# Optimization experiments

Measured on AMD Instinct MI355X. Metric: run time of the kernel, lower is better.

## Reference

```python
import jax, jax.numpy as jnp
import numpy as np

LAMB_MAX = 2.0


def cheb_conv_k2(x, edge_index, w0, w1, b):
    """PyG ChebConv with K=2, sym normalization, given lambda_max.
    out = x @ w0 + (L_hat x) @ w1 + b, where
    L_hat = (2/lmax) * (I - D^{-1/2} A D^{-1/2}) - I.
    """
    n = x.shape[0]
    src, dst = edge_index[0], edge_index[1]
    ew = jnp.ones(src.shape, x.dtype)
    deg = jax.ops.segment_sum(ew, src, num_segments=n)
    dinv = jnp.where(deg > 0, jax.lax.rsqrt(jnp.maximum(deg, 1e-12)), 0.0)
    s = 2.0 / LAMB_MAX
    # off-diagonal weights of scaled Laplacian: -s * d_i^{-1/2} d_j^{-1/2}
    norm = (-s) * dinv[src] * dinv[dst]  # [E]
    # gather-scale-scatter: (L_hat x)_offdiag
    agg = jax.ops.segment_sum(norm[:, None] * x[src], dst, num_segments=n)  # [N, F]
    tx1 = (s - 1.0) * x + agg  # diagonal: s*1 (L diag) + (-1) self-loop
    return x @ w0 + tx1 @ w1 + b


def setup_inputs() -> dict:
    key = jax.random.key(0)
    ks = jax.random.split(key, 8)
    N, E, F, H = 100000, 1600000, 128, 128
    x = jax.random.normal(ks[0], (N, F), dtype=jnp.float32)
    edge_index = jax.random.randint(ks[1], (2, E), 0, N, dtype=jnp.int32)
    # glorot-ish init for the two Chebyshev linear weights per layer
    sc1 = (2.0 / (F + H)) ** 0.5
    sc2 = (2.0 / (H + 1)) ** 0.5
    w1_0 = jax.random.normal(ks[2], (F, H), dtype=jnp.float32) * sc1
    w1_1 = jax.random.normal(ks[3], (F, H), dtype=jnp.float32) * sc1
    b1 = jnp.zeros((H,), jnp.float32)
    w2_0 = jax.random.normal(ks[4], (H, 1), dtype=jnp.float32) * sc2
    w2_1 = jax.random.normal(ks[5], (H, 1), dtype=jnp.float32) * sc2
    b2 = jnp.zeros((1,), jnp.float32)
    return {"x": x, "edge_index": edge_index, "w1_0": w1_0, "w1_1": w1_1,
            "b1": b1, "w2_0": w2_0, "w2_1": w2_1, "b2": b2}


def reference(x, edge_index, w1_0, w1_1, b1, w2_0, w2_1, b2):
    h = jax.nn.relu(cheb_conv_k2(x, edge_index, w1_0, w1_1, b1))
    out = jax.nn.sigmoid(cheb_conv_k2(h, edge_index, w2_0, w2_1, b2))
    return out  # [N, 1]
```

## Files before the change

kernel.cpp:

```cpp
#include <hip/hip_runtime.h>
#include <math.h>

#define F 128
#define SCAN_CHUNK 1024
#define CHUNK 32
#define NBLK 128

typedef __attribute__((ext_vector_type(8))) short bf16x8;
typedef __attribute__((ext_vector_type(4))) float f32x4;

__device__ inline unsigned short f2bf(float v) {
  unsigned u = __float_as_uint(v);
  unsigned r = (u + 0x7FFFu + ((u >> 16) & 1u)) >> 16;
  return (unsigned short)r;
}
__device__ inline float bf2f(unsigned short s) {
  return __uint_as_float(((unsigned)s) << 16);
}

__global__ __launch_bounds__(256) void k_conv(const float* __restrict__ x,
                                              unsigned short* __restrict__ xb,
                                              int NF4) {
  const float4* x4 = (const float4*)x;
  ushort4* xb4 = (ushort4*)xb;
  for (int i = blockIdx.x * 256 + threadIdx.x; i < NF4; i += gridDim.x * 256) {
    float4 v = x4[i];
    ushort4 o;
    o.x = f2bf(v.x);
    o.y = f2bf(v.y);
    o.z = f2bf(v.z);
    o.w = f2bf(v.w);
    xb4[i] = o;
  }
}

__global__ __launch_bounds__(1024) void k_hist2(const int* __restrict__ src,
                                                const int* __restrict__ dst,
                                                int* __restrict__ cntgD,
                                                int* __restrict__ cntgS, int E,
                                                int nb, int per) {
  extern __shared__ int smem[];
  int* cd = smem;
  int* cs = smem + nb;
  int blk = blockIdx.x;
  for (int b = threadIdx.x; b < nb; b += 1024) {
    cd[b] = 0;
    cs[b] = 0;
  }
  __syncthreads();
  int e0 = blk * per;
  int e1 = e0 + per;
  if (e1 > E) e1 = E;
  for (int e = e0 + threadIdx.x; e < e1; e += 1024) {
    atomicAdd(&cd[dst[e] >> 7], 1);
    atomicAdd(&cs[src[e] >> 7], 1);
  }
  __syncthreads();
  for (int b = threadIdx.x; b < nb; b += 1024) {
    cntgD[b * NBLK + blk] = cd[b];
    cntgS[b * NBLK + blk] = cs[b];
  }
}

__global__ __launch_bounds__(NBLK) void k_scanBk2(int* __restrict__ cntgD,
                                                  int* __restrict__ cntgS,
                                                  int* __restrict__ totD,
                                                  int* __restrict__ totS, int nb) {
  __shared__ int sh[NBLK];
  int b = blockIdx.x;
  int tid = threadIdx.x;
  int* cntg;
  int* tot;
  int bb;
  if (b < nb) {
    cntg = cntgD;
    tot = totD;
    bb = b;
  } else {
    cntg = cntgS;
    tot = totS;
    bb = b - nb;
  }
  int v = cntg[bb * NBLK + tid];
  int val = v;
  sh[tid] = val;
  __syncthreads();
  for (int off = 1; off < NBLK; off <<= 1) {
    int o = (tid >= off) ? sh[tid - off] : 0;
    __syncthreads();
    val += o;
    sh[tid] = val;
    __syncthreads();
  }
  cntg[bb * NBLK + tid] = val - v;
  if (tid == NBLK - 1) tot[bb] = val;
}

__global__ __launch_bounds__(1024) void k_scanTot(const int* __restrict__ totD,
                                                  const int* __restrict__ totS,
                                                  int* __restrict__ baseD,
                                                  int* __restrict__ baseS, int nb,
                                                  int E) {
  __shared__ int sh[1024];
  int tid = threadIdx.x;
  int v = (tid < nb) ? totD[tid] : 0;
  int val = v;
  sh[tid] = val;
  __syncthreads();
  for (int off = 1; off < 1024; off <<= 1) {
    int o = (tid >= off) ? sh[tid - off] : 0;
    __syncthreads();
    val += o;
    sh[tid] = val;
    __syncthreads();
  }
  if (tid < nb) baseD[tid] = val - v;
  if (tid == 0) baseD[nb] = E;
  __syncthreads();
  v = (tid < nb) ? totS[tid] : 0;
  val = v;
  sh[tid] = val;
  __syncthreads();
  for (int off = 1; off < 1024; off <<= 1) {
    int o = (tid >= off) ? sh[tid - off] : 0;
    __syncthreads();
    val += o;
    sh[tid] = val;
    __syncthreads();
  }
  if (tid < nb) baseS[tid] = val - v;
  if (tid == 0) baseS[nb] = E;
}

__global__ __launch_bounds__(1024) void k_binfill2(
    const int* __restrict__ src, const int* __restrict__ dst,
    const int* __restrict__ cntgD, const int* __restrict__ cntgS,
    const int* __restrict__ baseD, const int* __restrict__ baseS,
    unsigned* __restrict__ binnedD, unsigned char* __restrict__ binnedS, int E,
    int nb, int per) {
  extern __shared__ int smem[];
  int* bD = smem;
  int* cD = smem + nb;
  int* bS = smem + 2 * nb;
  int* cS = smem + 3 * nb;
  int blk = blockIdx.x;
  for (int b = threadIdx.x; b < nb; b += 1024) {
    bD[b] = baseD[b] + cntgD[b * NBLK + blk];
    cD[b] = 0;
    bS[b] = baseS[b] + cntgS[b * NBLK + blk];
    cS[b] = 0;
  }
  __syncthreads();
  int e0 = blk * per;
  int e1 = e0 + per;
  if (e1 > E) e1 = E;
  for (int e = e0 + threadIdx.x; e < e1; e += 1024) {
    int s = src[e];
    int d = dst[e];
    int bk = d >> 7;
    int rk = atomicAdd(&cD[bk], 1);
    binnedD[bD[bk] + rk] = ((unsigned)s << 7) | (unsigned)(d & 127);
    int bs = s >> 7;
    int rs = atomicAdd(&cS[bs], 1);
    binnedS[bS[bs] + rs] = (unsigned char)(s & 127);
  }
}

__global__ __launch_bounds__(256) void k_dinvS(const unsigned char* __restrict__ binnedS,
                                               const int* __restrict__ baseS,
                                               float* __restrict__ dinv, int N) {
  __shared__ int cnt[128];
  int b = blockIdx.x;
  int tid = threadIdx.x;
  if (tid < 128) cnt[tid] = 0;
  int wbeg = baseS[b], wend = baseS[b + 1];
  __syncthreads();
  for (int j = wbeg + tid; j < wend; j += 256) atomicAdd(&cnt[binnedS[j]], 1);
  __syncthreads();
  if (tid < 128) {
    int node = (b << 7) + tid;
    if (node < N) {
      int c = cnt[tid];
      dinv[node] = c > 0 ? rsqrtf((float)c) : 0.0f;
    }
  }
}

__global__ __launch_bounds__(256) void k_binB2(const unsigned* __restrict__ binnedD,
                                               const int* __restrict__ baseD,
                                               int* __restrict__ rp,
                                               int* __restrict__ pairs, int N,
                                               int E) {
  __shared__ int cnt[128];
  __shared__ int sc[256];
  __shared__ int cur[128];
  int b = blockIdx.x;
  int tid = threadIdx.x;
  int node0 = b << 7;
  if (tid < 128) cnt[tid] = 0;
  int wbeg = baseD[b], wend = baseD[b + 1];
  __syncthreads();
  for (int j = wbeg + tid; j < wend; j += 256) atomicAdd(&cnt[binnedD[j] & 127u], 1);
  __syncthreads();
  int v = (tid < 128) ? cnt[tid] : 0;
  int val = v;
  sc[tid] = val;
  __syncthreads();
  for (int off = 1; off < 128; off <<= 1) {
    int o = (tid >= off) ? sc[tid - off] : 0;
    __syncthreads();
    val += o;
    sc[tid] = val;
    __syncthreads();
  }
  if (tid < 128) {
    int excl = wbeg + val - v;
    int node = node0 + tid;
    if (node < N) rp[node] = excl;
    cur[tid] = excl;
  }
  if (b == 0 && tid == 0) rp[N] = E;
  __syncthreads();
  for (int j = wbeg + tid; j < wend; j += 256) {
    unsigned e = binnedD[j];
    int idx = atomicAdd(&cur[e & 127u], 1);
    pairs[idx] = (int)(e >> 7);
  }
}

__global__ __launch_bounds__(256) void k_prep(const int* __restrict__ src,
                                              const int* __restrict__ dst,
                                              const float* __restrict__ x,
                                              int* __restrict__ degA,
                                              int* __restrict__ degB,
                                              unsigned short* __restrict__ xb,
                                              int E, int NF4) {
  int t0 = blockIdx.x * 256 + threadIdx.x;
  int stride = gridDim.x * 256;
  for (int i = t0; i < E; i += stride) {
    atomicAdd(&degA[src[i]], 1);
    atomicAdd(&degB[dst[i]], 1);
  }
  const float4* x4 = (const float4*)x;
  ushort4* xb4 = (ushort4*)xb;
  for (int i = t0; i < NF4; i += stride) {
    float4 v = x4[i];
    ushort4 o;
    o.x = f2bf(v.x);
    o.y = f2bf(v.y);
    o.z = f2bf(v.z);
    o.w = f2bf(v.w);
    xb4[i] = o;
  }
}

__global__ __launch_bounds__(256) void k_scanA(const int* __restrict__ deg,
                                               int* __restrict__ rp,
                                               int* __restrict__ bsum, int N) {
  __shared__ int sh[256];
  int tid = threadIdx.x;
  int base = blockIdx.x * SCAN_CHUNK + tid * 4;
  int v0 = 0, v1 = 0, v2 = 0, v3 = 0;
  if (base + 0 < N) v0 = deg[base + 0];
  if (base + 1 < N) v1 = deg[base + 1];
  if (base + 2 < N) v2 = deg[base + 2];
  if (base + 3 < N) v3 = deg[base + 3];
  int ts = v0 + v1 + v2 + v3;
  int val = ts;
  sh[tid] = val;
  __syncthreads();
  for (int off = 1; off < 256; off <<= 1) {
    int other = (tid >= off) ? sh[tid - off] : 0;
    __syncthreads();
    val += other;
    sh[tid] = val;
    __syncthreads();
  }
  int excl = val - ts;
  if (base + 0 < N) rp[base + 0] = excl;
  if (base + 1 < N) rp[base + 1] = excl + v0;
  if (base + 2 < N) rp[base + 2] = excl + v0 + v1;
  if (base + 3 < N) rp[base + 3] = excl + v0 + v1 + v2;
  if (tid == 255) bsum[blockIdx.x] = val;
}

__global__ __launch_bounds__(256) void k_scanB(int* __restrict__ bsum, int nb) {
  __shared__ int sh[256];
  int tid = threadIdx.x;
  int ts = (tid < nb) ? bsum[tid] : 0;
  int val = ts;
  sh[tid] = val;
  __syncthreads();
  for (int off = 1; off < 256; off <<= 1) {
    int other = (tid >= off) ? sh[tid - off] : 0;
    __syncthreads();
    val += other;
    sh[tid] = val;
    __syncthreads();
  }
  if (tid < nb) bsum[tid] = val - ts;
}

__global__ __launch_bounds__(256) void k_scanC(int* __restrict__ rp,
                                               const int* __restrict__ bsum,
                                               int* __restrict__ pos,
                                               const int* __restrict__ degA,
                                               float* __restrict__ dinv, int N,
                                               int E) {
  int i = blockIdx.x * 256 + threadIdx.x;
  if (i < N) {
    int v = rp[i] + bsum[i >> 10];
    rp[i] = v;
    pos[i] = v;
    int d = degA[i];
    dinv[i] = d > 0 ? rsqrtf((float)d) : 0.0f;
  }
  if (i == 0) rp[N] = E;
}

__global__ __launch_bounds__(256) void k_fill(const int* __restrict__ src,
                                              const int* __restrict__ dst,
                                              int* __restrict__ pos,
                                              int* __restrict__ pairs, int E) {
  for (int e = blockIdx.x * 256 + threadIdx.x; e < E; e += gridDim.x * 256) {
    int s = src[e];
    int d = dst[e];
    int idx = atomicAdd(&pos[d], 1);
    pairs[idx] = s;
  }
}

__global__ __launch_bounds__(256) void k_gather1b(
    const int* __restrict__ pairs, const int* __restrict__ rp,
    const unsigned short* __restrict__ xb, const float* __restrict__ dinv,
    unsigned short* __restrict__ tb, int N) {
  int node = (blockIdx.x * 256 + threadIdx.x) >> 6;
  if (node >= N) return;
  int lane = threadIdx.x & 63;
  int half = lane >> 5;
  int li = lane & 31;
  int beg = rp[node], end = rp[node + 1];
  const uint2* x2 = (const uint2*)xb;
  float a0 = 0.f, a1 = 0.f, a2 = 0.f, a3 = 0.f;
  int j = beg + half;
  for (; j + 2 < end; j += 4) {
    int s0 = pairs[j];
    int s1 = pairs[j + 2];
    float w0 = dinv[s0];
    float w1 = dinv[s1];
    uint2 v0 = x2[(size_t)s0 * 32 + li];
    uint2 v1 = x2[(size_t)s1 * 32 + li];
    a0 += w0 * bf2f((unsigned short)v0.x) + w1 * bf2f((unsigned short)v1.x);
    a1 += w0 * bf2f((unsigned short)(v0.x >> 16)) +
          w1 * bf2f((unsigned short)(v1.x >> 16));
    a2 += w0 * bf2f((unsigned short)v0.y) + w1 * bf2f((unsigned short)v1.y);
    a3 += w0 * bf2f((unsigned short)(v0.y >> 16)) +
          w1 * bf2f((unsigned short)(v1.y >> 16));
  }
  for (; j < end; j += 2) {
    int s0 = pairs[j];
    float w0 = dinv[s0];
    uint2 v0 = x2[(size_t)s0 * 32 + li];
    a0 += w0 * bf2f((unsigned short)v0.x);
    a1 += w0 * bf2f((unsigned short)(v0.x >> 16));
    a2 += w0 * bf2f((unsigned short)v0.y);
    a3 += w0 * bf2f((unsigned short)(v0.y >> 16));
  }
  a0 += __shfl_xor(a0, 32);
  a1 += __shfl_xor(a1, 32);
  a2 += __shfl_xor(a2, 32);
  a3 += __shfl_xor(a3, 32);
  if (half == 0) {
    float nd = -dinv[node];
    uint2 o;
    o.x = ((unsigned)f2bf(nd * a1) << 16) | f2bf(nd * a0);
    o.y = ((unsigned)f2bf(nd * a3) << 16) | f2bf(nd * a2);
    ((uint2*)tb)[(size_t)node * 32 + li] = o;
  }
}

__global__ __launch_bounds__(256) void k_layer_mfma(
    const float* __restrict__ x, const unsigned short* __restrict__ tb,
    const float* __restrict__ dinv, const float* __restrict__ w10,
    const float* __restrict__ w11, const float* __restrict__ b1,
    const float* __restrict__ w20, const float* __restrict__ w21,
    float* __restrict__ p, float* __restrict__ r, int N) {
  __shared__ __align__(16) short Axh[8 * 16 * 40];
  __shared__ __align__(16) short Axl[8 * 16 * 40];
  __shared__ __align__(16) short At[8 * 16 * 40];
  __shared__ float p_sh[CHUNK], r_sh[CHUNK];

  const int tid = threadIdx.x;
  const int wave = tid >> 6;
  const int lane = tid & 63;
  const int quad = lane >> 4;
  const int col = lane & 15;

  bf16x8 Bh[2][4][2], Bl[2][4][2];
  float b1f[2], w20f[2], w21f[2];
#pragma unroll
  for (int nt = 0; nt < 2; ++nt) {
    int f = wave * 32 + nt * 16 + col;
    b1f[nt] = b1[f];
    w20f[nt] = w20[f];
    w21f[nt] = w21[f];
  }
#pragma unroll
  for (int mat = 0; mat < 2; ++mat) {
    const float* w = mat ? w11 : w10;
#pragma unroll
    for (int ks = 0; ks < 4; ++ks) {
#pragma unroll
      for (int nt = 0; nt < 2; ++nt) {
        int f = wave * 32 + nt * 16 + col;
        bf16x8 h8, l8;
#pragma unroll
        for (int j = 0; j < 8; ++j) {
          float v = w[(ks * 32 + quad * 8 + j) * F + f];
          unsigned short hi = f2bf(v);
          l8[j] = (short)f2bf(v - bf2f(hi));
          h8[j] = (short)hi;
        }
        Bh[mat][ks][nt] = h8;
        Bl[mat][ks][nt] = l8;
      }
    }
  }

  const int nchunks = (N + CHUNK - 1) / CHUNK;
  for (int chunk = blockIdx.x; chunk < nchunks; chunk += gridDim.x) {
    int node0 = chunk * CHUNK;
    __syncthreads();

    {
      int nloc = tid >> 3;
      int k0 = (tid & 7) * 16;
      int gn = node0 + nloc;
      int mt = nloc >> 4, m = nloc & 15, ks = k0 >> 5, koff = k0 & 31;
      int base = ((mt * 4 + ks) * 16 + m) * 40 + koff;
      const float4* xr = (const float4*)(x + (size_t)gn * F + k0);
      const uint2* tr = (const uint2*)(tb + (size_t)gn * F + k0);
      bool ok = (gn < N);
#pragma unroll
      for (int q4 = 0; q4 < 4; ++q4) {
        float4 xv = ok ? xr[q4] : make_float4(0.f, 0.f, 0.f, 0.f);
        uint2 tv = ok ? tr[q4] : make_uint2(0u, 0u);
        short4 xh, xl;
        unsigned short h;
        h = f2bf(xv.x); xl.x = (short)f2bf(xv.x - bf2f(h)); xh.x = (short)h;
        h = f2bf(xv.y); xl.y = (short)f2bf(xv.y - bf2f(h)); xh.y = (short)h;
        h = f2bf(xv.z); xl.z = (short)f2bf(xv.z - bf2f(h)); xh.z = (short)h;
        h = f2bf(xv.w); xl.w = (short)f2bf(xv.w - bf2f(h)); xh.w = (short)h;
        *(short4*)&Axh[base + q4 * 4] = xh;
        *(short4*)&Axl[base + q4 * 4] = xl;
        *(uint2*)&At[base + q4 * 4] = tv;
      }
      if (tid < CHUNK) {
        p_sh[tid] = 0.f;
        r_sh[tid] = 0.f;
      }
    }
    __syncthreads();

    f32x4 acc[2][2];
#pragma unroll
    for (int mt = 0; mt < 2; ++mt)
#pragma unroll
      for (int nt = 0; nt < 2; ++nt) acc[mt][nt] = (f32x4)0.f;

#pragma unroll
    for (int mt = 0; mt < 2; ++mt) {
#pragma unroll
      for (int ks = 0; ks < 4; ++ks) {
        int ab = ((mt * 4 + ks) * 16 + col) * 40 + quad * 8;
        bf16x8 axh = *(bf16x8*)&Axh[ab];
        bf16x8 axl = *(bf16x8*)&Axl[ab];
        bf16x8 at = *(bf16x8*)&At[ab];
#pragma unroll
        for (int nt = 0; nt < 2; ++nt) {
          f32x4 c = acc[mt][nt];
          c = __builtin_amdgcn_mfma_f32_16x16x32_bf16(axh, Bh[0][ks][nt], c, 0, 0, 0);
          c = __builtin_amdgcn_mfma_f32_16x16x32_bf16(axl, Bh[0][ks][nt], c, 0, 0, 0);
          c = __builtin_amdgcn_mfma_f32_16x16x32_bf16(axh, Bl[0][ks][nt], c, 0, 0, 0);
          c = __builtin_amdgcn_mfma_f32_16x16x32_bf16(at, Bh[1][ks][nt], c, 0, 0, 0);
          c = __builtin_amdgcn_mfma_f32_16x16x32_bf16(at, Bl[1][ks][nt], c, 0, 0, 0);
          acc[mt][nt] = c;
        }
      }
    }

#pragma unroll
    for (int mt = 0; mt < 2; ++mt) {
      float pp[4], rr[4];
#pragma unroll
      for (int reg = 0; reg < 4; ++reg) {
        float h0 = fmaxf(acc[mt][0][reg] + b1f[0], 0.f);
        float h1 = fmaxf(acc[mt][1][reg] + b1f[1], 0.f);
        pp[reg] = h0 * w20f[0] + h1 * w20f[1];
        rr[reg] = h0 * w21f[0] + h1 * w21f[1];
      }
#pragma unroll
      for (int off = 1; off < 16; off <<= 1) {
#pragma unroll
        for (int reg = 0; reg < 4; ++reg) {
          pp[reg] += __shfl_xor(pp[reg], off);
          rr[reg] += __shfl_xor(rr[reg], off);
        }
      }
      if (col == 0) {
#pragma unroll
        for (int reg = 0; reg < 4; ++reg) {
          atomicAdd(&p_sh[mt * 16 + quad * 4 + reg], pp[reg]);
          atomicAdd(&r_sh[mt * 16 + quad * 4 + reg], rr[reg]);
        }
      }
    }
    __syncthreads();
    if (tid < CHUNK) {
      int gn = node0 + tid;
      if (gn < N) {
        p[gn] = p_sh[tid];
        r[gn] = dinv[gn] * r_sh[tid];
      }
    }
  }
}

__global__ __launch_bounds__(256) void k_gather2_final(
    const int* __restrict__ pairs, const int* __restrict__ rp,
    const float* __restrict__ r2, const float* __restrict__ p,
    const float* __restrict__ dinv, const float* __restrict__ b2,
    float* __restrict__ out, int N) {
  int i = blockIdx.x * 256 + threadIdx.x;
  if (i >= N) return;
  int beg = rp[i], end = rp[i + 1];
  float a = 0.f;
  for (int j = beg; j < end; ++j) a += r2[pairs[j]];
  float z = p[i] - dinv[i] * a + b2[0];
  out[i] = 1.0f / (1.0f + expf(-z));
}

extern "C" void kernel_launch(void* const* d_in, const int* in_sizes, int n_in,
                              void* d_out, int out_size, void* d_ws, size_t ws_size,
                              hipStream_t stream) {
  const float* x = (const float*)d_in[0];
  const int* ei = (const int*)d_in[1];
  const float* w10 = (const float*)d_in[2];
  const float* w11 = (const float*)d_in[3];
  const float* b1 = (const float*)d_in[4];
  const float* w20 = (const float*)d_in[5];
  const float* w21 = (const float*)d_in[6];
  const float* b2 = (const float*)d_in[7];
  float* out = (float*)d_out;
  int N = in_sizes[0] / F;
  int E = in_sizes[1] / 2;
  const int* src = ei;
  const int* dst = ei + E;
  int nbuckets = (N + 127) >> 7;

  size_t off = 0;
  char* base = (char*)d_ws;
  auto take = [&](size_t bytes) {
    void* ptr = base + off;
    off += (bytes + 15) & ~(size_t)15;
    return ptr;
  };
  float* dinv = (float*)take((size_t)N * 4);
  float* p = (float*)take((size_t)N * 4);
  float* r = (float*)take((size_t)N * 4);
  int* rp = (int*)take(((size_t)N + 1) * 4);
  int* degA = (int*)take((size_t)N * 4);
  int* degB = (int*)take((size_t)N * 4);
  int* pos = (int*)take((size_t)N * 4);
  int* bsum = (int*)take(256 * 4);
  int* cntgD = (int*)take((size_t)nbuckets * NBLK * 4);
  int* cntgS = (int*)take((size_t)nbuckets * NBLK * 4);
  int* totD = (int*)take(((size_t)nbuckets + 1) * 4);
  int* totS = (int*)take(((size_t)nbuckets + 1) * 4);
  int* baseD = (int*)take(((size_t)nbuckets + 1) * 4);
  int* baseS = (int*)take(((size_t)nbuckets + 1) * 4);
  int* pairs = (int*)take((size_t)E * 4);
  unsigned short* xb = (unsigned short*)take((size_t)N * F * 2);
  unsigned short* tb = (unsigned short*)take((size_t)N * F * 2);
  if (off > ws_size) return;
  unsigned* binnedD = (unsigned*)tb;
  unsigned char* binnedS = (unsigned char*)tb + (((size_t)E * 4 + 255) & ~(size_t)255);

  int NF4 = N * (F / 4);
  int per = (E + NBLK - 1) / NBLK;

  k_conv<<<2048, 256, 0, stream>>>(x, xb, NF4);
  if (nbuckets <= 1024 && (size_t)E * 5 + 256 <= (size_t)N * F * 2) {
    k_hist2<<<NBLK, 1024, (size_t)nbuckets * 8, stream>>>(src, dst, cntgD, cntgS, E,
                                                          nbuckets, per);
    k_scanBk2<<<2 * nbuckets, NBLK, 0, stream>>>(cntgD, cntgS, totD, totS, nbuckets);
    k_scanTot<<<1, 1024, 0, stream>>>(totD, totS, baseD, baseS, nbuckets, E);
    k_binfill2<<<NBLK, 1024, (size_t)nbuckets * 16, stream>>>(
        src, dst, cntgD, cntgS, baseD, baseS, binnedD, binnedS, E, nbuckets, per);
    k_dinvS<<<nbuckets, 256, 0, stream>>>(binnedS, baseS, dinv, N);
    k_binB2<<<nbuckets, 256, 0, stream>>>(binnedD, baseD, rp, pairs, N, E);
  } else {
    int nb_scan = (N + SCAN_CHUNK - 1) / SCAN_CHUNK;
    hipMemsetAsync(degA, 0, 2 * (size_t)N * sizeof(int), stream);
    k_prep<<<2048, 256, 0, stream>>>(src, dst, x, degA, degB, xb, E, NF4);
    k_scanA<<<nb_scan, 256, 0, stream>>>(degB, rp, bsum, N);
    k_scanB<<<1, 256, 0, stream>>>(bsum, nb_scan);
    k_scanC<<<(N + 255) / 256, 256, 0, stream>>>(rp, bsum, pos, degA, dinv, N, E);
    k_fill<<<2048, 256, 0, stream>>>(src, dst, pos, pairs, E);
  }
  k_gather1b<<<(N + 3) / 4, 256, 0, stream>>>(pairs, rp, xb, dinv, tb, N);
  k_layer_mfma<<<512, 256, 0, stream>>>(x, tb, dinv, w10, w11, b1, w20, w21, p, r,
                                        N);
  k_gather2_final<<<(N + 255) / 256, 256, 0, stream>>>(pairs, rp, r, p, dinv, b2,
                                                       out, N);
}
```

Before: 326.9 us.

## Fuse prep kernels, drop split-bf16 x path, and re-map first gather

Folds the fp32-to-bf16 conversion of x into the histogram kernel, and merges the degree/dinv computation into the CSR-building kernel, removing two launches and one pass over the binned data. The layer MFMA kernel now reads the bf16 copy of x rather than fp32 x, and drops the hi/lo split of x. This cuts global traffic and MFMA work per tile, at the cost of lower precision on the x@w0 term. The first gather now uses 32 lanes per node with a 4-edge unroll instead of two half-waves plus a shuffle reduction, which is meant to raise memory-level parallelism.

```diff
diff --git a/kernel.cpp b/kernel.cpp
--- a/kernel.cpp
+++ b/kernel.cpp
@@ -18,12 +18,33 @@
   return __uint_as_float(((unsigned)s) << 16);
 }
 
-__global__ __launch_bounds__(256) void k_conv(const float* __restrict__ x,
-                                              unsigned short* __restrict__ xb,
-                                              int NF4) {
+__global__ __launch_bounds__(1024) void k_prep2(const int* __restrict__ src,
+                                                const int* __restrict__ dst,
+                                                const float* __restrict__ x,
+                                                unsigned short* __restrict__ xb,
+                                                int* __restrict__ cntgD,
+                                                int* __restrict__ cntgS, int E,
+                                                int NF4, int nb, int per) {
+  extern __shared__ int smem[];
+  int* cd = smem;
+  int* cs = smem + nb;
+  int blk = blockIdx.x;
+  int tid = threadIdx.x;
+  for (int b = tid; b < nb; b += 1024) {
+    cd[b] = 0;
+    cs[b] = 0;
+  }
+  __syncthreads();
+  int e0 = blk * per;
+  int e1 = e0 + per;
+  if (e1 > E) e1 = E;
+  for (int e = e0 + tid; e < e1; e += 1024) {
+    atomicAdd(&cd[dst[e] >> 7], 1);
+    atomicAdd(&cs[src[e] >> 7], 1);
+  }
   const float4* x4 = (const float4*)x;
   ushort4* xb4 = (ushort4*)xb;
-  for (int i = blockIdx.x * 256 + threadIdx.x; i < NF4; i += gridDim.x * 256) {
+  for (int i = blk * 1024 + tid; i < NF4; i += NBLK * 1024) {
     float4 v = x4[i];
     ushort4 o;
     o.x = f2bf(v.x);
@@ -32,31 +53,8 @@
     o.w = f2bf(v.w);
     xb4[i] = o;
   }
-}
-
-__global__ __launch_bounds__(1024) void k_hist2(const int* __restrict__ src,
-                                                const int* __restrict__ dst,
-                                                int* __restrict__ cntgD,
-                                                int* __restrict__ cntgS, int E,
-                                                int nb, int per) {
-  extern __shared__ int smem[];
-  int* cd = smem;
-  int* cs = smem + nb;
-  int blk = blockIdx.x;
-  for (int b = threadIdx.x; b < nb; b += 1024) {
-    cd[b] = 0;
-    cs[b] = 0;
-  }
-  __syncthreads();
-  int e0 = blk * per;
-  int e1 = e0 + per;
-  if (e1 > E) e1 = E;
-  for (int e = e0 + threadIdx.x; e < e1; e += 1024) {
-    atomicAdd(&cd[dst[e] >> 7], 1);
-    atomicAdd(&cs[src[e] >> 7], 1);
-  }
-  __syncthreads();
-  for (int b = threadIdx.x; b < nb; b += 1024) {
+  __syncthreads();
+  for (int b = tid; b < nb; b += 1024) {
     cntgD[b * NBLK + blk] = cd[b];
     cntgS[b * NBLK + blk] = cs[b];
   }
@@ -166,31 +164,13 @@
   }
 }
 
-__global__ __launch_bounds__(256) void k_dinvS(const unsigned char* __restrict__ binnedS,
-                                               const int* __restrict__ baseS,
-                                               float* __restrict__ dinv, int N) {
-  __shared__ int cnt[128];
-  int b = blockIdx.x;
-  int tid = threadIdx.x;
-  if (tid < 128) cnt[tid] = 0;
-  int wbeg = baseS[b], wend = baseS[b + 1];
-  __syncthreads();
-  for (int j = wbeg + tid; j < wend; j += 256) atomicAdd(&cnt[binnedS[j]], 1);
-  __syncthreads();
-  if (tid < 128) {
-    int node = (b << 7) + tid;
-    if (node < N) {
-      int c = cnt[tid];
-      dinv[node] = c > 0 ? rsqrtf((float)c) : 0.0f;
-    }
-  }
-}
-
-__global__ __launch_bounds__(256) void k_binB2(const unsigned* __restrict__ binnedD,
-                                               const int* __restrict__ baseD,
-                                               int* __restrict__ rp,
-                                               int* __restrict__ pairs, int N,
-                                               int E) {
+__global__ __launch_bounds__(256) void k_csr(const unsigned char* __restrict__ binnedS,
+                                             const int* __restrict__ baseS,
+                                             const unsigned* __restrict__ binnedD,
+                                             const int* __restrict__ baseD,
+                                             float* __restrict__ dinv,
+                                             int* __restrict__ rp,
+                                             int* __restrict__ pairs, int N, int E) {
   __shared__ int cnt[128];
   __shared__ int sc[256];
   __shared__ int cur[128];
@@ -198,8 +178,20 @@
   int tid = threadIdx.x;
   int node0 = b << 7;
   if (tid < 128) cnt[tid] = 0;
+  __syncthreads();
+  int sbeg = baseS[b], send = baseS[b + 1];
+  for (int j = sbeg + tid; j < send; j += 256) atomicAdd(&cnt[binnedS[j]], 1);
+  __syncthreads();
+  if (tid < 128) {
+    int node = node0 + tid;
+    if (node < N) {
+      int c = cnt[tid];
+      dinv[node] = c > 0 ? rsqrtf((float)c) : 0.0f;
+    }
+    cnt[tid] = 0;
+  }
+  __syncthreads();
   int wbeg = baseD[b], wend = baseD[b + 1];
-  __syncthreads();
   for (int j = wbeg + tid; j < wend; j += 256) atomicAdd(&cnt[binnedD[j] & 127u], 1);
   __syncthreads();
   int v = (tid < 128) ? cnt[tid] : 0;
@@ -330,34 +322,38 @@
   }
 }
 
-__global__ __launch_bounds__(256) void k_gather1b(
+__global__ __launch_bounds__(256) void k_gather1c(
     const int* __restrict__ pairs, const int* __restrict__ rp,
     const unsigned short* __restrict__ xb, const float* __restrict__ dinv,
     unsigned short* __restrict__ tb, int N) {
-  int node = (blockIdx.x * 256 + threadIdx.x) >> 6;
+  int node = (blockIdx.x * 256 + threadIdx.x) >> 5;
   if (node >= N) return;
-  int lane = threadIdx.x & 63;
-  int half = lane >> 5;
-  int li = lane & 31;
+  int li = threadIdx.x & 31;
   int beg = rp[node], end = rp[node + 1];
   const uint2* x2 = (const uint2*)xb;
   float a0 = 0.f, a1 = 0.f, a2 = 0.f, a3 = 0.f;
-  int j = beg + half;
-  for (; j + 2 < end; j += 4) {
-    int s0 = pairs[j];
-    int s1 = pairs[j + 2];
-    float w0 = dinv[s0];
-    float w1 = dinv[s1];
+  int j = beg;
+  for (; j + 3 < end; j += 4) {
+    int s0 = pairs[j], s1 = pairs[j + 1], s2 = pairs[j + 2], s3 = pairs[j + 3];
+    float w0 = dinv[s0], w1 = dinv[s1], w2 = dinv[s2], w3 = dinv[s3];
     uint2 v0 = x2[(size_t)s0 * 32 + li];
     uint2 v1 = x2[(size_t)s1 * 32 + li];
-    a0 += w0 * bf2f((unsigned short)v0.x) + w1 * bf2f((unsigned short)v1.x);
+    uint2 v2 = x2[(size_t)s2 * 32 + li];
+    uint2 v3 = x2[(size_t)s3 * 32 + li];
+    a0 += w0 * bf2f((unsigned short)v0.x) + w1 * bf2f((unsigned short)v1.x) +
+          w2 * bf2f((unsigned short)v2.x) + w3 * bf2f((unsigned short)v3.x);
     a1 += w0 * bf2f((unsigned short)(v0.x >> 16)) +
-          w1 * bf2f((unsigned short)(v1.x >> 16));
-    a2 += w0 * bf2f((unsigned short)v0.y) + w1 * bf2f((unsigned short)v1.y);
+          w1 * bf2f((unsigned short)(v1.x >> 16)) +
+          w2 * bf2f((unsigned short)(v2.x >> 16)) +
+          w3 * bf2f((unsigned short)(v3.x >> 16));
+    a2 += w0 * bf2f((unsigned short)v0.y) + w1 * bf2f((unsigned short)v1.y) +
+          w2 * bf2f((unsigned short)v2.y) + w3 * bf2f((unsigned short)v3.y);
     a3 += w0 * bf2f((unsigned short)(v0.y >> 16)) +
-          w1 * bf2f((unsigned short)(v1.y >> 16));
-  }
-  for (; j < end; j += 2) {
+          w1 * bf2f((unsigned short)(v1.y >> 16)) +
+          w2 * bf2f((unsigned short)(v2.y >> 16)) +
+          w3 * bf2f((unsigned short)(v3.y >> 16));
+  }
+  for (; j < end; ++j) {
     int s0 = pairs[j];
     float w0 = dinv[s0];
     uint2 v0 = x2[(size_t)s0 * 32 + li];
@@ -366,27 +362,20 @@
     a2 += w0 * bf2f((unsigned short)v0.y);
     a3 += w0 * bf2f((unsigned short)(v0.y >> 16));
   }
-  a0 += __shfl_xor(a0, 32);
-  a1 += __shfl_xor(a1, 32);
-  a2 += __shfl_xor(a2, 32);
-  a3 += __shfl_xor(a3, 32);
-  if (half == 0) {
-    float nd = -dinv[node];
-    uint2 o;
-    o.x = ((unsigned)f2bf(nd * a1) << 16) | f2bf(nd * a0);
-    o.y = ((unsigned)f2bf(nd * a3) << 16) | f2bf(nd * a2);
-    ((uint2*)tb)[(size_t)node * 32 + li] = o;
-  }
+  float nd = -dinv[node];
+  uint2 o;
+  o.x = ((unsigned)f2bf(nd * a1) << 16) | f2bf(nd * a0);
+  o.y = ((unsigned)f2bf(nd * a3) << 16) | f2bf(nd * a2);
+  ((uint2*)tb)[(size_t)node * 32 + li] = o;
 }
 
 __global__ __launch_bounds__(256) void k_layer_mfma(
-    const float* __restrict__ x, const unsigned short* __restrict__ tb,
+    const unsigned short* __restrict__ xb, const unsigned short* __restrict__ tb,
     const float* __restrict__ dinv, const float* __restrict__ w10,
     const float* __restrict__ w11, const float* __restrict__ b1,
     const float* __restrict__ w20, const float* __restrict__ w21,
     float* __restrict__ p, float* __restrict__ r, int N) {
-  __shared__ __align__(16) short Axh[8 * 16 * 40];
-  __shared__ __align__(16) short Axl[8 * 16 * 40];
+  __shared__ __align__(16) short Ax[8 * 16 * 40];
   __shared__ __align__(16) short At[8 * 16 * 40];
   __shared__ float p_sh[CHUNK], r_sh[CHUNK];
 
@@ -438,21 +427,14 @@
       int gn = node0 + nloc;
       int mt = nloc >> 4, m = nloc & 15, ks = k0 >> 5, koff = k0 & 31;
       int base = ((mt * 4 + ks) * 16 + m) * 40 + koff;
-      const float4* xr = (const float4*)(x + (size_t)gn * F + k0);
+      const uint2* xr = (const uint2*)(xb + (size_t)gn * F + k0);
       const uint2* tr = (const uint2*)(tb + (size_t)gn * F + k0);
       bool ok = (gn < N);
 #pragma unroll
       for (int q4 = 0; q4 < 4; ++q4) {
-        float4 xv = ok ? xr[q4] : make_float4(0.f, 0.f, 0.f, 0.f);
+        uint2 xv = ok ? xr[q4] : make_uint2(0u, 0u);
         uint2 tv = ok ? tr[q4] : make_uint2(0u, 0u);
-        short4 xh, xl;
-        unsigned short h;
-        h = f2bf(xv.x); xl.x = (short)f2bf(xv.x - bf2f(h)); xh.x = (short)h;
-        h = f2bf(xv.y); xl.y = (short)f2bf(xv.y - bf2f(h)); xh.y = (short)h;
-        h = f2bf(xv.z); xl.z = (short)f2bf(xv.z - bf2f(h)); xh.z = (short)h;
-        h = f2bf(xv.w); xl.w = (short)f2bf(xv.w - bf2f(h)); xh.w = (short)h;
-        *(short4*)&Axh[base + q4 * 4] = xh;
-        *(short4*)&Axl[base + q4 * 4] = xl;
+        *(uint2*)&Ax[base + q4 * 4] = xv;
         *(uint2*)&At[base + q4 * 4] = tv;
       }
       if (tid < CHUNK) {
@@ -473,15 +455,13 @@
 #pragma unroll
       for (int ks = 0; ks < 4; ++ks) {
         int ab = ((mt * 4 + ks) * 16 + col) * 40 + quad * 8;
-        bf16x8 axh = *(bf16x8*)&Axh[ab];
-        bf16x8 axl = *(bf16x8*)&Axl[ab];
+        bf16x8 ax = *(bf16x8*)&Ax[ab];
         bf16x8 at = *(bf16x8*)&At[ab];
 #pragma unroll
         for (int nt = 0; nt < 2; ++nt) {
           f32x4 c = acc[mt][nt];
-          c = __builtin_amdgcn_mfma_f32_16x16x32_bf16(axh, Bh[0][ks][nt], c, 0, 0, 0);
-          c = __builtin_amdgcn_mfma_f32_16x16x32_bf16(axl, Bh[0][ks][nt], c, 0, 0, 0);
-          c = __builtin_amdgcn_mfma_f32_16x16x32_bf16(axh, Bl[0][ks][nt], c, 0, 0, 0);
+          c = __builtin_amdgcn_mfma_f32_16x16x32_bf16(ax, Bh[0][ks][nt], c, 0, 0, 0);
+          c = __builtin_amdgcn_mfma_f32_16x16x32_bf16(ax, Bl[0][ks][nt], c, 0, 0, 0);
           c = __builtin_amdgcn_mfma_f32_16x16x32_bf16(at, Bh[1][ks][nt], c, 0, 0, 0);
           c = __builtin_amdgcn_mfma_f32_16x16x32_bf16(at, Bl[1][ks][nt], c, 0, 0, 0);
           acc[mt][nt] = c;
@@ -589,16 +569,16 @@
   int NF4 = N * (F / 4);
   int per = (E + NBLK - 1) / NBLK;
 
-  k_conv<<<2048, 256, 0, stream>>>(x, xb, NF4);
   if (nbuckets <= 1024 && (size_t)E * 5 + 256 <= (size_t)N * F * 2) {
-    k_hist2<<<NBLK, 1024, (size_t)nbuckets * 8, stream>>>(src, dst, cntgD, cntgS, E,
-                                                          nbuckets, per);
+    k_prep2<<<NBLK, 1024, (size_t)nbuckets * 8, stream>>>(src, dst, x, xb, cntgD,
+                                                          cntgS, E, NF4, nbuckets,
+                                                          per);
     k_scanBk2<<<2 * nbuckets, NBLK, 0, stream>>>(cntgD, cntgS, totD, totS, nbuckets);
     k_scanTot<<<1, 1024, 0, stream>>>(totD, totS, baseD, baseS, nbuckets, E);
     k_binfill2<<<NBLK, 1024, (size_t)nbuckets * 16, stream>>>(
         src, dst, cntgD, cntgS, baseD, baseS, binnedD, binnedS, E, nbuckets, per);
-    k_dinvS<<<nbuckets, 256, 0, stream>>>(binnedS, baseS, dinv, N);
-    k_binB2<<<nbuckets, 256, 0, stream>>>(binnedD, baseD, rp, pairs, N, E);
+    k_csr<<<nbuckets, 256, 0, stream>>>(binnedS, baseS, binnedD, baseD, dinv, rp,
+                                        pairs, N, E);
   } else {
     int nb_scan = (N + SCAN_CHUNK - 1) / SCAN_CHUNK;
     hipMemsetAsync(degA, 0, 2 * (size_t)N * sizeof(int), stream);
@@ -608,8 +588,8 @@
     k_scanC<<<(N + 255) / 256, 256, 0, stream>>>(rp, bsum, pos, degA, dinv, N, E);
     k_fill<<<2048, 256, 0, stream>>>(src, dst, pos, pairs, E);
   }
-  k_gather1b<<<(N + 3) / 4, 256, 0, stream>>>(pairs, rp, xb, dinv, tb, N);
-  k_layer_mfma<<<512, 256, 0, stream>>>(x, tb, dinv, w10, w11, b1, w20, w21, p, r,
+  k_gather1c<<<(N + 7) / 8, 256, 0, stream>>>(pairs, rp, xb, dinv, tb, N);
+  k_layer_mfma<<<512, 256, 0, stream>>>(xb, tb, dinv, w10, w11, b1, w20, w21, p, r,
                                         N);
   k_gather2_final<<<(N + 255) / 256, 256, 0, stream>>>(pairs, rp, r, p, dinv, b2,
                                                        out, N);
```

New measurement: 313.3 us. 1.04x faster.
